# Kernel optimization log

Hardware: AMD Instinct MI355X
Metric: run time of the kernel (lower is better)

## Reference

```python
import jax, jax.numpy as jnp
import numpy as np

COLB = 16            # COL_BLOCK_WIDTH
IN_W = 1024          # input_width; zero_inputs=0 so input_locations = arange(IN_W)
OUT_W = 512          # output_width
DEPTH = 8            # network_depth
IN_L = 4             # butterfly_in_depth
OUT_L = 4            # butterfly_out_depth
ACT = 8              # activations_per_block
BLOCKS = 64          # blocks_per_layer -> num_inputs = 1024 per module
CURV = 1.0
GROW = BLOCKS * ACT  # 512 new rows per module
TOTAL = IN_W + DEPTH * GROW  # 5120
BATCH = 4096


def setup_inputs() -> dict:
    key = jax.random.key(0)
    k1, k2, k3 = jax.random.split(key, 3)
    input_data = jax.random.normal(k1, (IN_W, BATCH), dtype=jnp.float32)
    scales = jnp.full((IN_W,), 0.05, dtype=jnp.float32)
    # angles uniform in (-pi, pi), shape [depth, in_layers+out_layers, num_inputs/2]
    angles = (jax.random.uniform(k2, (DEPTH, IN_L + OUT_L, BLOCKS * COLB // 2)) * 2.0 - 1.0) * np.pi
    angles = angles.astype(jnp.float32)
    biases = jax.random.normal(k3, (DEPTH, GROW), dtype=jnp.float32) * 0.05
    # per-module indices_in = randperm(total_width_so_far)[:num_inputs]
    rng = np.random.RandomState(0)
    tw = IN_W
    idxs = []
    for _ in range(DEPTH):
        idxs.append(rng.permutation(tw)[: BLOCKS * COLB].astype(np.int32))
        tw += GROW
    indices_in = jnp.asarray(np.stack(idxs))  # [depth, 1024]
    return {"input_data": input_data, "scales": scales, "angles": angles,
            "biases": biases, "indices_in": indices_in}


def _rotate(x, ang, stride):
    # x: [W, B]; pair row i (with (i//stride)%2==0) with row i+stride inside 16-blocks
    W, B = x.shape
    xr = x.reshape(W // (2 * stride), 2, stride, B)
    a = ang.reshape(W // (2 * stride), stride)[:, :, None]
    c, s = jnp.cos(a), jnp.sin(a)
    lo, hi = xr[:, 0], xr[:, 1]              # [W/2s, s, B]
    nlo = c * lo + s * hi
    nhi = -s * lo + c * hi
    return jnp.stack([nlo, nhi], axis=1).reshape(W, B)


def _butterfly_module(data, ang, bias, idx, idx_out):
    W = BLOCKS * COLB
    x = data[idx]                             # gather [1024, B]
    for l in range(IN_L):
        x = _rotate(x, ang[l], 2 ** (l % 4))
    xb = x.reshape(BLOCKS, COLB, -1)
    pre = xb[:, :ACT, :] + bias.reshape(BLOCKS, ACT)[:, :, None]
    # curvature (smoothed-ReLU) activation
    act = 0.5 * (pre + jnp.sqrt(pre * pre + CURV * CURV))
    xb = xb.at[:, :ACT, :].set(act)
    x = xb.reshape(W, -1)
    for l in range(OUT_L):
        x = _rotate(x, ang[IN_L + l], 2 ** ((IN_L + l) % 4))
    data = data.at[idx].set(x)                # scatter working set back
    data = data.at[idx_out: idx_out + GROW].set(act.reshape(GROW, -1))
    return data


def reference(input_data, scales, angles, biases, indices_in):
    B = input_data.shape[1]
    data = jnp.zeros((TOTAL, B), dtype=input_data.dtype)
    data = data.at[:IN_W].set(scales[:, None] * input_data)
    for i in range(DEPTH):
        data = _butterfly_module(data, angles[i], biases[i], indices_in[i], IN_W + GROW * i)
    return data[TOTAL - OUT_W:]
```

## Files before the change

kernel.cpp:

```cpp
#include <hip/hip_runtime.h>
#include <math.h>

#define N_INW     1024
#define N_DEPTH   8
#define N_GROW    512
#define N_BATCH   4096
#define N_THREADS 64
#define N_LAYERS  64

typedef __attribute__((ext_vector_type(2))) float F2;
typedef decltype(__builtin_amdgcn_cvt_pkrtz(0.f, 0.f)) H2;

__global__ void precompute_kernel(const float* __restrict__ angles,
                                  const int*   __restrict__ indices,
                                  float* __restrict__ cs,
                                  int*   __restrict__ addrs) {
    int i = blockIdx.x * blockDim.x + threadIdx.x;
    if (i < N_LAYERS * 512) {
        int g = i >> 9, p = i & 511;
        float a = angles[i];
        cs[g * 1024 + p]       = cosf(a);
        cs[g * 1024 + 512 + p] = sinf(a);
    }
    if (i < N_DEPTH * N_INW) {
        int v = indices[i];
        addrs[i] = (v + (v >> 4)) << 2;
    }
}

#define ADDR(r) ((((r) + ((r) >> 4))) << 2)

#define LD2(A) ({ H2 _h = *(const H2*)(L + (A));                               \
                  F2 _v; _v.x = (float)_h.x; _v.y = (float)_h.y; _v; })
#define ST2(A, V) do { F2 _w = (V);                                            \
    *(H2*)(L + (A)) = __builtin_amdgcn_cvt_pkrtz(_w.x, _w.y); } while (0)

#define LDCS_K(K, CA, CB, SA, SB) do { if (USE_TABLE) {                        \
    const float4* _c = (const float4*)(csb + (K)*1024 + (blk<<3));             \
    const float4* _s = (const float4*)(csb + (K)*1024 + 512 + (blk<<3));       \
    CA = _c[0]; CB = _c[1]; SA = _s[0]; SB = _s[1];                            \
  } else {                                                                     \
    const float4* _p = (const float4*)(anb + (K)*512 + (blk<<3));              \
    float4 _a = _p[0], _b = _p[1];                                             \
    __sincosf(_a.x, &SA.x, &CA.x); __sincosf(_a.y, &SA.y, &CA.y);              \
    __sincosf(_a.z, &SA.z, &CA.z); __sincosf(_a.w, &SA.w, &CA.w);              \
    __sincosf(_b.x, &SB.x, &CB.x); __sincosf(_b.y, &SB.y, &CB.y);              \
    __sincosf(_b.z, &SB.z, &CB.z); __sincosf(_b.w, &SB.w, &CB.w);              \
  } } while (0)

#define TR(v) (((v) + ((v) >> 4)) << 2)
#define LDADDR_P(PA, PI) do { if (USE_TABLE) {                                 \
    const int4* _ip = (const int4*)((PA) + (blk<<4));                          \
    i0 = _ip[0]; i1 = _ip[1]; i2 = _ip[2]; i3 = _ip[3];                        \
  } else {                                                                     \
    const int4* _ip = (const int4*)((PI) + (blk<<4));                          \
    int4 _v0=_ip[0], _v1=_ip[1], _v2=_ip[2], _v3=_ip[3];                       \
    i0.x=TR(_v0.x); i0.y=TR(_v0.y); i0.z=TR(_v0.z); i0.w=TR(_v0.w);            \
    i1.x=TR(_v1.x); i1.y=TR(_v1.y); i1.z=TR(_v1.z); i1.w=TR(_v1.w);            \
    i2.x=TR(_v2.x); i2.y=TR(_v2.y); i2.z=TR(_v2.z); i2.w=TR(_v2.w);            \
    i3.x=TR(_v3.x); i3.y=TR(_v3.y); i3.z=TR(_v3.z); i3.w=TR(_v3.w);            \
  } } while (0)

#define ROTP(LO, HI, CC, SS) do { F2 _l = LO, _h = HI;                         \
    LO = CC * _l + SS * _h; HI = CC * _h - SS * _l; } while (0)

#define ROTS1(CA,CB,SA,SB) do {                                                \
    ROTP(x0,x1,CA.x,SA.x);  ROTP(x2,x3,CA.y,SA.y);                             \
    ROTP(x4,x5,CA.z,SA.z);  ROTP(x6,x7,CA.w,SA.w);                             \
    ROTP(x8,x9,CB.x,SB.x);  ROTP(x10,x11,CB.y,SB.y);                           \
    ROTP(x12,x13,CB.z,SB.z);ROTP(x14,x15,CB.w,SB.w); } while (0)
#define ROTS2(CA,CB,SA,SB) do {                                                \
    ROTP(x0,x2,CA.x,SA.x);  ROTP(x1,x3,CA.y,SA.y);                             \
    ROTP(x4,x6,CA.z,SA.z);  ROTP(x5,x7,CA.w,SA.w);                             \
    ROTP(x8,x10,CB.x,SB.x); ROTP(x9,x11,CB.y,SB.y);                            \
    ROTP(x12,x14,CB.z,SB.z);ROTP(x13,x15,CB.w,SB.w); } while (0)
#define ROTS4(CA,CB,SA,SB) do {                                                \
    ROTP(x0,x4,CA.x,SA.x);  ROTP(x1,x5,CA.y,SA.y);                             \
    ROTP(x2,x6,CA.z,SA.z);  ROTP(x3,x7,CA.w,SA.w);                             \
    ROTP(x8,x12,CB.x,SB.x); ROTP(x9,x13,CB.y,SB.y);                            \
    ROTP(x10,x14,CB.z,SB.z);ROTP(x11,x15,CB.w,SB.w); } while (0)
#define ROTS8(CA,CB,SA,SB) do {                                                \
    ROTP(x0,x8,CA.x,SA.x);  ROTP(x1,x9,CA.y,SA.y);                             \
    ROTP(x2,x10,CA.z,SA.z); ROTP(x3,x11,CA.w,SA.w);                            \
    ROTP(x4,x12,CB.x,SB.x); ROTP(x5,x13,CB.y,SB.y);                            \
    ROTP(x6,x14,CB.z,SB.z); ROTP(x7,x15,CB.w,SB.w); } while (0)

#define ACT1(X, BB) do { F2 _p = (X) + (BB);                                   \
    F2 _t = _p * _p + 1.0f;                                                    \
    F2 _r; _r.x = __builtin_amdgcn_sqrtf(_t.x);                                \
    _r.y = __builtin_amdgcn_sqrtf(_t.y);                                       \
    X = 0.5f * (_p + _r); } while (0)

#define FENCE() __builtin_amdgcn_sched_barrier(0)

#define GATHER()                                                               \
  const int a0=i0.x, a1=i0.y, a2=i0.z, a3=i0.w, a4=i1.x, a5=i1.y,              \
            a6=i1.z, a7=i1.w, a8=i2.x, a9=i2.y, a10=i2.z, a11=i2.w,            \
            a12=i3.x, a13=i3.y, a14=i3.z, a15=i3.w;                            \
  F2 x0=LD2(a0), x1=LD2(a1), x2=LD2(a2), x3=LD2(a3),                           \
     x4=LD2(a4), x5=LD2(a5), x6=LD2(a6), x7=LD2(a7),                           \
     x8=LD2(a8), x9=LD2(a9), x10=LD2(a10), x11=LD2(a11),                       \
     x12=LD2(a12), x13=LD2(a13), x14=LD2(a14), x15=LD2(a15);

template <bool USE_TABLE>
__global__ __launch_bounds__(N_THREADS, 2)
void butterfly_fused_kernel(const float* __restrict__ input,
                            const float* __restrict__ scales,
                            const float* __restrict__ biases,
                            const int*   __restrict__ indices,
                            const float* __restrict__ cs_tab,
                            const int*   __restrict__ addr_tab,
                            const float* __restrict__ angles,
                            float* __restrict__ out) {
    extern __shared__ float ldsbuf[];
    char* L = (char*)ldsbuf;
    const int blk = threadIdx.x;
    const int b   = blockIdx.x;
    const int cg  = (((b & 7) * 256) + (b >> 3)) * 2;

    float4 ca0,cb0,sa0,sb0, ca1,cb1,sa1,sb1, ca2,cb2,sa2,sb2, ca3,cb3,sa3,sb3;
    float4 bA, bB;
    int4 i0, i1, i2, i3;

    const float* csb = cs_tab;
    const float* anb = angles;
    const int*   atb = addr_tab + N_INW;
    const int*   inb = indices + N_INW;
    const float* bnb = biases + N_GROW;

    LDADDR_P(addr_tab, indices);
    LDCS_K(0, ca0,cb0,sa0,sb0);
    LDCS_K(1, ca1,cb1,sa1,sb1);
    LDCS_K(2, ca2,cb2,sa2,sb2);
    LDCS_K(3, ca3,cb3,sa3,sb3);
    { const float4* bp = (const float4*)(biases + (blk << 3));
      bA = bp[0]; bB = bp[1]; }

#pragma unroll
    for (int k = 0; k < 16; ++k) {
        const int r = (k << 6) + blk;
        F2 v = *(const F2*)(input + (size_t)r * N_BATCH + cg);
        ST2(ADDR(r), scales[r] * v);
    }

#pragma unroll 1
    for (int m = 0; m < 7; ++m) {
        GATHER();
        float4 da0,db0,ta0,tb0, da1,db1,ta1,tb1, da2,db2,ta2,tb2, da3,db3,ta3,tb3;
        LDCS_K(4, da0,db0,ta0,tb0);
        LDCS_K(5, da1,db1,ta1,tb1);
        LDCS_K(6, da2,db2,ta2,tb2);
        LDCS_K(7, da3,db3,ta3,tb3);
        FENCE();
        ROTS1(ca0,cb0,sa0,sb0);
        ROTS2(ca1,cb1,sa1,sb1);
        ROTS4(ca2,cb2,sa2,sb2);
        ROTS8(ca3,cb3,sa3,sb3);
        ACT1(x0,bA.x); ACT1(x1,bA.y); ACT1(x2,bA.z); ACT1(x3,bA.w);
        ACT1(x4,bB.x); ACT1(x5,bB.y); ACT1(x6,bB.z); ACT1(x7,bB.w);
        const int br = N_INW + m * N_GROW + (blk << 3);
        const int ab = ADDR(br);
        ST2(ab+ 0,x0); ST2(ab+ 4,x1); ST2(ab+ 8,x2); ST2(ab+12,x3);
        ST2(ab+16,x4); ST2(ab+20,x5); ST2(ab+24,x6); ST2(ab+28,x7);
        LDCS_K(8,  ca0,cb0,sa0,sb0);
        LDCS_K(9,  ca1,cb1,sa1,sb1);
        LDCS_K(10, ca2,cb2,sa2,sb2);
        LDCS_K(11, ca3,cb3,sa3,sb3);
        LDADDR_P(atb, inb);
        { const float4* bp = (const float4*)(bnb + (blk << 3));
          bA = bp[0]; bB = bp[1]; }
        FENCE();
        ROTS1(da0,db0,ta0,tb0);
        ROTS2(da1,db1,ta1,tb1);
        ROTS4(da2,db2,ta2,tb2);
        ROTS8(da3,db3,ta3,tb3);
        ST2(a0,x0);  ST2(a1,x1);  ST2(a2,x2);  ST2(a3,x3);
        ST2(a4,x4);  ST2(a5,x5);  ST2(a6,x6);  ST2(a7,x7);
        ST2(a8,x8);  ST2(a9,x9);  ST2(a10,x10); ST2(a11,x11);
        ST2(a12,x12); ST2(a13,x13); ST2(a14,x14); ST2(a15,x15);
        csb += 8192; anb += 4096; atb += N_INW; inb += N_INW; bnb += N_GROW;
    }

    {
        GATHER();
        FENCE();
        ROTS1(ca0,cb0,sa0,sb0);
        ROTS2(ca1,cb1,sa1,sb1);
        ROTS4(ca2,cb2,sa2,sb2);
        ROTS8(ca3,cb3,sa3,sb3);
        ACT1(x0,bA.x); ACT1(x1,bA.y); ACT1(x2,bA.z); ACT1(x3,bA.w);
        ACT1(x4,bB.x); ACT1(x5,bB.y); ACT1(x6,bB.z); ACT1(x7,bB.w);
        *(F2*)(out + (size_t)((blk<<3)+0)*N_BATCH + cg) = x0;
        *(F2*)(out + (size_t)((blk<<3)+1)*N_BATCH + cg) = x1;
        *(F2*)(out + (size_t)((blk<<3)+2)*N_BATCH + cg) = x2;
        *(F2*)(out + (size_t)((blk<<3)+3)*N_BATCH + cg) = x3;
        *(F2*)(out + (size_t)((blk<<3)+4)*N_BATCH + cg) = x4;
        *(F2*)(out + (size_t)((blk<<3)+5)*N_BATCH + cg) = x5;
        *(F2*)(out + (size_t)((blk<<3)+6)*N_BATCH + cg) = x6;
        *(F2*)(out + (size_t)((blk<<3)+7)*N_BATCH + cg) = x7;
    }
}

extern "C" void kernel_launch(void* const* d_in, const int* in_sizes, int n_in,
                              void* d_out, int out_size, void* d_ws, size_t ws_size,
                              hipStream_t stream) {
    const float* input   = (const float*)d_in[0];
    const float* scales  = (const float*)d_in[1];
    const float* angles  = (const float*)d_in[2];
    const float* biases  = (const float*)d_in[3];
    const int*   indices = (const int*)d_in[4];
    float* out = (float*)d_out;

    const size_t cs_bytes  = (size_t)N_LAYERS * 2 * 512 * sizeof(float);
    const size_t adr_bytes = (size_t)N_DEPTH * N_INW * sizeof(int);
    const size_t lds_bytes = (size_t)4608 * 4 + 288 * 4;
    const int grid = N_BATCH / 2;

    if (ws_size >= cs_bytes + adr_bytes) {
        float* cs  = (float*)d_ws;
        int* addrs = (int*)((char*)d_ws + cs_bytes);
        precompute_kernel<<<N_LAYERS * 512 / 256, 256, 0, stream>>>(angles, indices, cs, addrs);
        butterfly_fused_kernel<true><<<grid, N_THREADS, lds_bytes, stream>>>(
            input, scales, biases, indices, cs, addrs, angles, out);
    } else {
        butterfly_fused_kernel<false><<<grid, N_THREADS, lds_bytes, stream>>>(
            input, scales, biases, indices, nullptr, nullptr, angles, out);
    }
}
```

Baseline: 104.6 us.

## Pack cos/sin tables as fp16 and double-buffer next-module coefficients in registers

The precompute kernel now stores cos/sin as interleaved fp16 per 8-pair block, so each layer's coefficients for a thread arrive in two 16-byte loads instead of four. The main loop is restructured into ping-pong A/B register sets. All 8 layers' coefficients, indices and biases for the next module are prefetched while the current module computes. This halves table traffic and hides global load latency across module boundaries, at the cost of higher register pressure and fp16 rounding of the rotation coefficients.

```diff
diff --git a/kernel.cpp b/kernel.cpp
--- a/kernel.cpp
+++ b/kernel.cpp
@@ -13,14 +13,15 @@
 
 __global__ void precompute_kernel(const float* __restrict__ angles,
                                   const int*   __restrict__ indices,
-                                  float* __restrict__ cs,
+                                  _Float16* __restrict__ csh,
                                   int*   __restrict__ addrs) {
     int i = blockIdx.x * blockDim.x + threadIdx.x;
     if (i < N_LAYERS * 512) {
-        int g = i >> 9, p = i & 511;
+        int g = i >> 9, p = i & 511, blk = p >> 3, j = p & 7;
         float a = angles[i];
-        cs[g * 1024 + p]       = cosf(a);
-        cs[g * 1024 + 512 + p] = sinf(a);
+        _Float16* base = csh + g * 1024 + blk * 16;
+        base[j]     = (_Float16)cosf(a);
+        base[8 + j] = (_Float16)sinf(a);
     }
     if (i < N_DEPTH * N_INW) {
         int v = indices[i];
@@ -35,31 +36,61 @@
 #define ST2(A, V) do { F2 _w = (V);                                            \
     *(H2*)(L + (A)) = __builtin_amdgcn_cvt_pkrtz(_w.x, _w.y); } while (0)
 
-#define LDCS_K(K, CA, CB, SA, SB) do { if (USE_TABLE) {                        \
-    const float4* _c = (const float4*)(csb + (K)*1024 + (blk<<3));             \
-    const float4* _s = (const float4*)(csb + (K)*1024 + 512 + (blk<<3));       \
-    CA = _c[0]; CB = _c[1]; SA = _s[0]; SB = _s[1];                            \
+#define PKU(x, y) __builtin_bit_cast(unsigned int,                             \
+                      __builtin_amdgcn_cvt_pkrtz((x), (y)))
+
+#define UNPK(Q, FA, FB) do {                                                   \
+    H2 _h0 = __builtin_bit_cast(H2, (Q).x), _h1 = __builtin_bit_cast(H2, (Q).y),\
+       _h2 = __builtin_bit_cast(H2, (Q).z), _h3 = __builtin_bit_cast(H2, (Q).w);\
+    FA.x = (float)_h0.x; FA.y = (float)_h0.y; FA.z = (float)_h1.x;             \
+    FA.w = (float)_h1.y; FB.x = (float)_h2.x; FB.y = (float)_h2.y;             \
+    FB.z = (float)_h3.x; FB.w = (float)_h3.y; } while (0)
+
+#define DECL_SET(P)                                                            \
+    uint4 P##c0, P##s0, P##c1, P##s1, P##c2, P##s2, P##c3, P##s3,              \
+          P##c4, P##s4, P##c5, P##s5, P##c6, P##s6, P##c7, P##s7;              \
+    int4  P##i0, P##i1, P##i2, P##i3;                                          \
+    float4 P##bA, P##bB;
+
+#define SYN1(P, K, ANB) do {                                                   \
+    const float4* _p = (const float4*)((ANB) + (K)*512 + (blk << 3));          \
+    float4 _u = _p[0], _v = _p[1];                                             \
+    float _c0,_c1,_c2,_c3,_c4,_c5,_c6,_c7,_t0,_t1,_t2,_t3,_t4,_t5,_t6,_t7;     \
+    __sincosf(_u.x,&_t0,&_c0); __sincosf(_u.y,&_t1,&_c1);                      \
+    __sincosf(_u.z,&_t2,&_c2); __sincosf(_u.w,&_t3,&_c3);                      \
+    __sincosf(_v.x,&_t4,&_c4); __sincosf(_v.y,&_t5,&_c5);                      \
+    __sincosf(_v.z,&_t6,&_c6); __sincosf(_v.w,&_t7,&_c7);                      \
+    P##c##K = make_uint4(PKU(_c0,_c1),PKU(_c2,_c3),PKU(_c4,_c5),PKU(_c6,_c7)); \
+    P##s##K = make_uint4(PKU(_t0,_t1),PKU(_t2,_t3),PKU(_t4,_t5),PKU(_t6,_t7)); \
+  } while (0)
+
+#define LOADCS1(P, K, CSN, ANB) do { if (USE_TABLE) {                          \
+    const char* _b = (CSN) + (blk << 5) + (K)*2048;                            \
+    P##c##K = *(const uint4*)(_b); P##s##K = *(const uint4*)(_b + 16);         \
+  } else { SYN1(P, K, ANB); } } while (0)
+
+#define LOADCS8(P, CSN, ANB) do {                                              \
+    LOADCS1(P,0,CSN,ANB); LOADCS1(P,1,CSN,ANB); LOADCS1(P,2,CSN,ANB);          \
+    LOADCS1(P,3,CSN,ANB); LOADCS1(P,4,CSN,ANB); LOADCS1(P,5,CSN,ANB);          \
+    LOADCS1(P,6,CSN,ANB); LOADCS1(P,7,CSN,ANB); } while (0)
+#define LOADCS4(P, CSN, ANB) do {                                              \
+    LOADCS1(P,0,CSN,ANB); LOADCS1(P,1,CSN,ANB); LOADCS1(P,2,CSN,ANB);          \
+    LOADCS1(P,3,CSN,ANB); } while (0)
+
+#define TR(v) (((v) + ((v) >> 4)) << 2)
+#define LOAD_AB(P, ATN, INB, BIN) do { if (USE_TABLE) {                        \
+    const int4* _ip = (const int4*)((ATN) + (blk << 4));                       \
+    P##i0=_ip[0]; P##i1=_ip[1]; P##i2=_ip[2]; P##i3=_ip[3];                    \
   } else {                                                                     \
-    const float4* _p = (const float4*)(anb + (K)*512 + (blk<<3));              \
-    float4 _a = _p[0], _b = _p[1];                                             \
-    __sincosf(_a.x, &SA.x, &CA.x); __sincosf(_a.y, &SA.y, &CA.y);              \
-    __sincosf(_a.z, &SA.z, &CA.z); __sincosf(_a.w, &SA.w, &CA.w);              \
-    __sincosf(_b.x, &SB.x, &CB.x); __sincosf(_b.y, &SB.y, &CB.y);              \
-    __sincosf(_b.z, &SB.z, &CB.z); __sincosf(_b.w, &SB.w, &CB.w);              \
-  } } while (0)
-
-#define TR(v) (((v) + ((v) >> 4)) << 2)
-#define LDADDR_P(PA, PI) do { if (USE_TABLE) {                                 \
-    const int4* _ip = (const int4*)((PA) + (blk<<4));                          \
-    i0 = _ip[0]; i1 = _ip[1]; i2 = _ip[2]; i3 = _ip[3];                        \
-  } else {                                                                     \
-    const int4* _ip = (const int4*)((PI) + (blk<<4));                          \
+    const int4* _ip = (const int4*)((INB) + (blk << 4));                       \
     int4 _v0=_ip[0], _v1=_ip[1], _v2=_ip[2], _v3=_ip[3];                       \
-    i0.x=TR(_v0.x); i0.y=TR(_v0.y); i0.z=TR(_v0.z); i0.w=TR(_v0.w);            \
-    i1.x=TR(_v1.x); i1.y=TR(_v1.y); i1.z=TR(_v1.z); i1.w=TR(_v1.w);            \
-    i2.x=TR(_v2.x); i2.y=TR(_v2.y); i2.z=TR(_v2.z); i2.w=TR(_v2.w);            \
-    i3.x=TR(_v3.x); i3.y=TR(_v3.y); i3.z=TR(_v3.z); i3.w=TR(_v3.w);            \
-  } } while (0)
+    P##i0.x=TR(_v0.x); P##i0.y=TR(_v0.y); P##i0.z=TR(_v0.z); P##i0.w=TR(_v0.w);\
+    P##i1.x=TR(_v1.x); P##i1.y=TR(_v1.y); P##i1.z=TR(_v1.z); P##i1.w=TR(_v1.w);\
+    P##i2.x=TR(_v2.x); P##i2.y=TR(_v2.y); P##i2.z=TR(_v2.z); P##i2.w=TR(_v2.w);\
+    P##i3.x=TR(_v3.x); P##i3.y=TR(_v3.y); P##i3.z=TR(_v3.z); P##i3.w=TR(_v3.w);\
+  }                                                                            \
+  const float4* _bp = (const float4*)((BIN) + (blk << 3));                     \
+  P##bA = _bp[0]; P##bB = _bp[1]; } while (0)
 
 #define ROTP(LO, HI, CC, SS) do { F2 _l = LO, _h = HI;                         \
     LO = CC * _l + SS * _h; HI = CC * _h - SS * _l; } while (0)
@@ -85,6 +116,10 @@
     ROTP(x4,x12,CB.x,SB.x); ROTP(x5,x13,CB.y,SB.y);                            \
     ROTP(x6,x14,CB.z,SB.z); ROTP(x7,x15,CB.w,SB.w); } while (0)
 
+#define ROTL(P, K, ROTM) do { float4 _CA,_CB,_SA,_SB;                          \
+    UNPK(P##c##K, _CA, _CB); UNPK(P##s##K, _SA, _SB);                          \
+    ROTM(_CA,_CB,_SA,_SB); } while (0)
+
 #define ACT1(X, BB) do { F2 _p = (X) + (BB);                                   \
     F2 _t = _p * _p + 1.0f;                                                    \
     F2 _r; _r.x = __builtin_amdgcn_sqrtf(_t.x);                                \
@@ -93,14 +128,32 @@
 
 #define FENCE() __builtin_amdgcn_sched_barrier(0)
 
-#define GATHER()                                                               \
-  const int a0=i0.x, a1=i0.y, a2=i0.z, a3=i0.w, a4=i1.x, a5=i1.y,              \
-            a6=i1.z, a7=i1.w, a8=i2.x, a9=i2.y, a10=i2.z, a11=i2.w,            \
-            a12=i3.x, a13=i3.y, a14=i3.z, a15=i3.w;                            \
+#define PROC_MOD(P, N, CSN, ANN, ATN, INB, BIN, M, FULL) do {                  \
+  const int a0=P##i0.x, a1=P##i0.y, a2=P##i0.z, a3=P##i0.w,                    \
+            a4=P##i1.x, a5=P##i1.y, a6=P##i1.z, a7=P##i1.w,                    \
+            a8=P##i2.x, a9=P##i2.y, a10=P##i2.z, a11=P##i2.w,                  \
+            a12=P##i3.x, a13=P##i3.y, a14=P##i3.z, a15=P##i3.w;                \
   F2 x0=LD2(a0), x1=LD2(a1), x2=LD2(a2), x3=LD2(a3),                           \
      x4=LD2(a4), x5=LD2(a5), x6=LD2(a6), x7=LD2(a7),                           \
      x8=LD2(a8), x9=LD2(a9), x10=LD2(a10), x11=LD2(a11),                       \
-     x12=LD2(a12), x13=LD2(a13), x14=LD2(a14), x15=LD2(a15);
+     x12=LD2(a12), x13=LD2(a13), x14=LD2(a14), x15=LD2(a15);                   \
+  if (FULL) { LOADCS8(N, CSN, ANN); } else { LOADCS4(N, CSN, ANN); }           \
+  FENCE();                                                                     \
+                     \
+  ROTL(P,0,ROTS1); ROTL(P,1,ROTS2); ROTL(P,2,ROTS4); ROTL(P,3,ROTS8);          \
+  ACT1(x0,P##bA.x); ACT1(x1,P##bA.y); ACT1(x2,P##bA.z); ACT1(x3,P##bA.w);      \
+  ACT1(x4,P##bB.x); ACT1(x5,P##bB.y); ACT1(x6,P##bB.z); ACT1(x7,P##bB.w);      \
+  const int _ab = ADDR(N_INW + (M)*N_GROW + (blk << 3));                       \
+  ST2(_ab+ 0,x0); ST2(_ab+ 4,x1); ST2(_ab+ 8,x2); ST2(_ab+12,x3);              \
+  ST2(_ab+16,x4); ST2(_ab+20,x5); ST2(_ab+24,x6); ST2(_ab+28,x7);              \
+  LOAD_AB(N, ATN, INB, BIN);                                                   \
+  FENCE();                                                                     \
+  ROTL(P,4,ROTS1); ROTL(P,5,ROTS2); ROTL(P,6,ROTS4); ROTL(P,7,ROTS8);          \
+  ST2(a0,x0);  ST2(a1,x1);  ST2(a2,x2);  ST2(a3,x3);                           \
+  ST2(a4,x4);  ST2(a5,x5);  ST2(a6,x6);  ST2(a7,x7);                           \
+  ST2(a8,x8);  ST2(a9,x9);  ST2(a10,x10); ST2(a11,x11);                        \
+  ST2(a12,x12); ST2(a13,x13); ST2(a14,x14); ST2(a15,x15);                      \
+} while (0)
 
 template <bool USE_TABLE>
 __global__ __launch_bounds__(N_THREADS, 2)
@@ -108,7 +161,7 @@
                             const float* __restrict__ scales,
                             const float* __restrict__ biases,
                             const int*   __restrict__ indices,
-                            const float* __restrict__ cs_tab,
+                            const char*  __restrict__ cs_tab,
                             const int*   __restrict__ addr_tab,
                             const float* __restrict__ angles,
                             float* __restrict__ out) {
@@ -118,23 +171,10 @@
     const int b   = blockIdx.x;
     const int cg  = (((b & 7) * 256) + (b >> 3)) * 2;
 
-    float4 ca0,cb0,sa0,sb0, ca1,cb1,sa1,sb1, ca2,cb2,sa2,sb2, ca3,cb3,sa3,sb3;
-    float4 bA, bB;
-    int4 i0, i1, i2, i3;
-
-    const float* csb = cs_tab;
-    const float* anb = angles;
-    const int*   atb = addr_tab + N_INW;
-    const int*   inb = indices + N_INW;
-    const float* bnb = biases + N_GROW;
-
-    LDADDR_P(addr_tab, indices);
-    LDCS_K(0, ca0,cb0,sa0,sb0);
-    LDCS_K(1, ca1,cb1,sa1,sb1);
-    LDCS_K(2, ca2,cb2,sa2,sb2);
-    LDCS_K(3, ca3,cb3,sa3,sb3);
-    { const float4* bp = (const float4*)(biases + (blk << 3));
-      bA = bp[0]; bB = bp[1]; }
+    DECL_SET(A) DECL_SET(B)
+
+    LOADCS8(A, cs_tab, angles);
+    LOAD_AB(A, addr_tab, indices, biases);
 
 #pragma unroll
     for (int k = 0; k < 16; ++k) {
@@ -143,53 +183,33 @@
         ST2(ADDR(r), scales[r] * v);
     }
 
+    const char*  csn = cs_tab + 16384;
+    const float* ann = angles + 4096;
+    const int*   atn = addr_tab + N_INW;
+    const int*   inb = indices + N_INW;
+    const float* bin = biases + N_GROW;
+
 #pragma unroll 1
-    for (int m = 0; m < 7; ++m) {
-        GATHER();
-        float4 da0,db0,ta0,tb0, da1,db1,ta1,tb1, da2,db2,ta2,tb2, da3,db3,ta3,tb3;
-        LDCS_K(4, da0,db0,ta0,tb0);
-        LDCS_K(5, da1,db1,ta1,tb1);
-        LDCS_K(6, da2,db2,ta2,tb2);
-        LDCS_K(7, da3,db3,ta3,tb3);
+    for (int t = 0; t < 3; ++t) {
+        const int m = 2 * t;
+        PROC_MOD(A, B, csn, ann, atn, inb, bin, m, 1);
+        csn += 16384; ann += 4096; atn += N_INW; inb += N_INW; bin += N_GROW;
+        PROC_MOD(B, A, csn, ann, atn, inb, bin, m + 1, 1);
+        csn += 16384; ann += 4096; atn += N_INW; inb += N_INW; bin += N_GROW;
+    }
+    PROC_MOD(A, B, csn, ann, atn, inb, bin, 6, 0);
+
+    {
+        const int a0=Bi0.x, a1=Bi0.y, a2=Bi0.z, a3=Bi0.w,
+                  a4=Bi1.x, a5=Bi1.y, a6=Bi1.z, a7=Bi1.w;
+        F2 x0=LD2(a0), x1=LD2(a1), x2=LD2(a2), x3=LD2(a3),
+           x4=LD2(a4), x5=LD2(a5), x6=LD2(a6), x7=LD2(a7);
+        F2 x8=LD2(Bi2.x), x9=LD2(Bi2.y), x10=LD2(Bi2.z), x11=LD2(Bi2.w),
+           x12=LD2(Bi3.x), x13=LD2(Bi3.y), x14=LD2(Bi3.z), x15=LD2(Bi3.w);
         FENCE();
-        ROTS1(ca0,cb0,sa0,sb0);
-        ROTS2(ca1,cb1,sa1,sb1);
-        ROTS4(ca2,cb2,sa2,sb2);
-        ROTS8(ca3,cb3,sa3,sb3);
-        ACT1(x0,bA.x); ACT1(x1,bA.y); ACT1(x2,bA.z); ACT1(x3,bA.w);
-        ACT1(x4,bB.x); ACT1(x5,bB.y); ACT1(x6,bB.z); ACT1(x7,bB.w);
-        const int br = N_INW + m * N_GROW + (blk << 3);
-        const int ab = ADDR(br);
-        ST2(ab+ 0,x0); ST2(ab+ 4,x1); ST2(ab+ 8,x2); ST2(ab+12,x3);
-        ST2(ab+16,x4); ST2(ab+20,x5); ST2(ab+24,x6); ST2(ab+28,x7);
-        LDCS_K(8,  ca0,cb0,sa0,sb0);
-        LDCS_K(9,  ca1,cb1,sa1,sb1);
-        LDCS_K(10, ca2,cb2,sa2,sb2);
-        LDCS_K(11, ca3,cb3,sa3,sb3);
-        LDADDR_P(atb, inb);
-        { const float4* bp = (const float4*)(bnb + (blk << 3));
-          bA = bp[0]; bB = bp[1]; }
-        FENCE();
-        ROTS1(da0,db0,ta0,tb0);
-        ROTS2(da1,db1,ta1,tb1);
-        ROTS4(da2,db2,ta2,tb2);
-        ROTS8(da3,db3,ta3,tb3);
-        ST2(a0,x0);  ST2(a1,x1);  ST2(a2,x2);  ST2(a3,x3);
-        ST2(a4,x4);  ST2(a5,x5);  ST2(a6,x6);  ST2(a7,x7);
-        ST2(a8,x8);  ST2(a9,x9);  ST2(a10,x10); ST2(a11,x11);
-        ST2(a12,x12); ST2(a13,x13); ST2(a14,x14); ST2(a15,x15);
-        csb += 8192; anb += 4096; atb += N_INW; inb += N_INW; bnb += N_GROW;
-    }
-
-    {
-        GATHER();
-        FENCE();
-        ROTS1(ca0,cb0,sa0,sb0);
-        ROTS2(ca1,cb1,sa1,sb1);
-        ROTS4(ca2,cb2,sa2,sb2);
-        ROTS8(ca3,cb3,sa3,sb3);
-        ACT1(x0,bA.x); ACT1(x1,bA.y); ACT1(x2,bA.z); ACT1(x3,bA.w);
-        ACT1(x4,bB.x); ACT1(x5,bB.y); ACT1(x6,bB.z); ACT1(x7,bB.w);
+        ROTL(B,0,ROTS1); ROTL(B,1,ROTS2); ROTL(B,2,ROTS4); ROTL(B,3,ROTS8);
+        ACT1(x0,BbA.x); ACT1(x1,BbA.y); ACT1(x2,BbA.z); ACT1(x3,BbA.w);
+        ACT1(x4,BbB.x); ACT1(x5,BbB.y); ACT1(x6,BbB.z); ACT1(x7,BbB.w);
         *(F2*)(out + (size_t)((blk<<3)+0)*N_BATCH + cg) = x0;
         *(F2*)(out + (size_t)((blk<<3)+1)*N_BATCH + cg) = x1;
         *(F2*)(out + (size_t)((blk<<3)+2)*N_BATCH + cg) = x2;
@@ -211,17 +231,18 @@
     const int*   indices = (const int*)d_in[4];
     float* out = (float*)d_out;
 
-    const size_t cs_bytes  = (size_t)N_LAYERS * 2 * 512 * sizeof(float);
+    const size_t cs_bytes  = (size_t)N_LAYERS * 2048;
     const size_t adr_bytes = (size_t)N_DEPTH * N_INW * sizeof(int);
     const size_t lds_bytes = (size_t)4608 * 4 + 288 * 4;
     const int grid = N_BATCH / 2;
 
     if (ws_size >= cs_bytes + adr_bytes) {
-        float* cs  = (float*)d_ws;
+        _Float16* csh = (_Float16*)d_ws;
         int* addrs = (int*)((char*)d_ws + cs_bytes);
-        precompute_kernel<<<N_LAYERS * 512 / 256, 256, 0, stream>>>(angles, indices, cs, addrs);
+        precompute_kernel<<<(N_LAYERS * 512 + 255) / 256, 256, 0, stream>>>(
+            angles, indices, csh, addrs);
         butterfly_fused_kernel<true><<<grid, N_THREADS, lds_bytes, stream>>>(
-            input, scales, biases, indices, cs, addrs, angles, out);
+            input, scales, biases, indices, (const char*)csh, addrs, angles, out);
     } else {
         butterfly_fused_kernel<false><<<grid, N_THREADS, lds_bytes, stream>>>(
             input, scales, biases, indices, nullptr, nullptr, angles, out);
```

Result: faster. 100.5 us (-3.9%).
